# Kernel optimization log

Hardware: AMD Instinct MI355X
Metric: run time of the kernel (lower is better)

The kernel has to match this reference:

```python
import jax, jax.numpy as jnp
import numpy as np

FACTOR = 0.2          # rotation/zoom/shift factor (init kwarg)
SCALE = 1.0 / 255.0   # rescale (init kwarg)
TWO_PI = 6.283185307179586
B, H, W, C = 64, 224, 224, 3


def _reflect(i, n):
    # TF fill_mode='reflect' index mapping (symmetric with edge repeat)
    m = jnp.mod(i, 2 * n)
    return jnp.where(m >= n, 2 * n - 1 - m, m)


def _bilinear(img, xs, ys):
    # img [H,W,C]; xs, ys [H,W] = input-space sample coords for each output pixel
    h, w, _ = img.shape
    x0f = jnp.floor(xs)
    y0f = jnp.floor(ys)
    fx = (xs - x0f)[..., None]
    fy = (ys - y0f)[..., None]
    x0 = x0f.astype(jnp.int32)
    y0 = y0f.astype(jnp.int32)
    x0r = _reflect(x0, w); x1r = _reflect(x0 + 1, w)
    y0r = _reflect(y0, h); y1r = _reflect(y0 + 1, h)
    Ia = img[y0r, x0r]; Ib = img[y0r, x1r]
    Ic = img[y1r, x0r]; Id = img[y1r, x1r]
    top = Ia * (1.0 - fx) + Ib * fx
    bot = Ic * (1.0 - fx) + Id * fx
    return top * (1.0 - fy) + bot * fy


_warp = jax.vmap(_bilinear)  # over batch: images [B,H,W,C], coords [B,H,W]


def setup_inputs() -> dict:
    key = jax.random.key(0)
    k = jax.random.split(key, 5)
    return {
        "image": jax.random.uniform(k[0], (B, H, W, C), jnp.float32) * 255.0,
        "angle_u": jax.random.uniform(k[1], (B,), jnp.float32),
        "zoom_u": jax.random.uniform(k[2], (B, 2), jnp.float32),
        "shift_u": jax.random.uniform(k[3], (B, 2), jnp.float32),
        "flip_u": jax.random.uniform(k[4], (B,), jnp.float32),
    }


def reference(image, angle_u, zoom_u, shift_u, flip_u):
    b, h, w, _ = image.shape
    dt = image.dtype
    yy, xx = jnp.meshgrid(jnp.arange(h, dtype=dt), jnp.arange(w, dtype=dt), indexing='ij')
    cx = (w - 1) / 2.0
    cy = (h - 1) / 2.0

    # 1) rescale
    x = image * SCALE

    # 2) random rotation: angle uniform in [-factor*2pi, +factor*2pi]
    theta = (2.0 * angle_u - 1.0) * FACTOR * TWO_PI            # [B]
    c = jnp.cos(theta)[:, None, None]
    s = jnp.sin(theta)[:, None, None]
    xr = c * (xx - cx) - s * (yy - cy) + cx                    # [B,H,W]
    yr = s * (xx - cx) + c * (yy - cy) + cy
    x = _warp(x, xr, yr)

    # 3) random zoom: zoom factor uniform in [1-factor, 1+factor] per axis
    z = 1.0 + (2.0 * zoom_u - 1.0) * FACTOR                    # [B,2] (h, w)
    zh = z[:, 0][:, None, None]
    zw = z[:, 1][:, None, None]
    xz = zw * (xx - cx) + cx
    yz = zh * (yy - cy) + cy
    x = _warp(x, xz, yz)

    # 4) random translation: shift fraction uniform in [-factor, factor]
    sh = (2.0 * shift_u - 1.0) * FACTOR                        # [B,2] (h, w)
    dy = (sh[:, 0] * h)[:, None, None]
    dx = (sh[:, 1] * w)[:, None, None]
    xt = xx - dx
    yt = yy - dy
    x = _warp(x, xt, yt)

    # 5) random horizontal flip (p = 0.5)
    flip = flip_u > 0.5
    x = jnp.where(flip[:, None, None, None], x[:, :, ::-1, :], x)
    return x
```

## Files before the change

kernel.cpp:

```cpp
#include <hip/hip_runtime.h>
#include <hip/hip_fp16.h>
#include <math.h>

#define BB 64
#define HH 224
#define WW 224
#define CC 3

constexpr float FACTOR  = 0.2f;
constexpr float SCALE_K = 1.0f / 255.0f;
constexpr float TWO_PI_F = 6.283185307179586f;
constexpr float CX = (WW - 1) * 0.5f;
constexpr float CY = (HH - 1) * 0.5f;
constexpr int PIX = HH * WW;
constexpr int IMG_ELEMS = PIX * CC;

constexpr int NXCD = 8;

constexpr int T2X = WW / 32;
constexpr int T2Y = HH / 16;
constexpr int TILES2 = T2X * T2Y;
constexpr int NBLOCKS2 = BB * TILES2;

constexpr int SZP = 50;
constexpr int ZP2 = 34;

typedef float f32x4 __attribute__((ext_vector_type(4), aligned(4)));
typedef float f32x2 __attribute__((ext_vector_type(2), aligned(4)));
typedef unsigned int u32x4 __attribute__((ext_vector_type(4), aligned(8)));

__device__ __forceinline__ int reflect1(int i, int n) {
    i = (i < 0) ? (-1 - i) : i;
    return (i >= n) ? (2 * n - 1 - i) : i;
}

__device__ __forceinline__ void rhull(int a, int b, int n, int& lo, int& hi) {
    int ra = reflect1(a, n), rb = reflect1(b, n);
    lo = min(ra, rb); hi = max(ra, rb);
    if (a <= 0 && b >= -1) lo = 0;
    if (b >= n - 1 && a <= n) hi = n - 1;
}

__device__ __forceinline__ float h2f(unsigned short u) {
    return __half2float(__ushort_as_half(u));
}

__device__ __forceinline__ void decode_tile32(int bid, int& b, int& ox, int& oy) {
    int xcd  = bid & (NXCD - 1);
    int slot = bid >> 3;
    int bi   = slot / TILES2;
    int t    = slot - bi * TILES2;
    b = xcd + bi * NXCD;
    int ty = t / T2X;
    int tx = t - ty * T2X;
    ox = tx * 32; oy = ty * 16;
}

__global__ __launch_bounds__(256)
void rotate_kernel(const float* __restrict__ image, uint2* __restrict__ tmp,
                   const float* __restrict__ angle_u) {
    int b, ox, oy;
    decode_tile32(blockIdx.x, b, ox, oy);
    const int lx = threadIdx.x & 31, ly = threadIdx.x >> 5;
    const int x = ox + lx;

    const float theta = (2.0f * angle_u[b] - 1.0f) * FACTOR * TWO_PI_F;
    const float c = __cosf(theta), s = __sinf(theta);
    const float rx = (float)x - CX;
    const float* img = image + (size_t)b * IMG_ELEMS;

    float fx[2], fy[2];
    bool sA[2], sB[2];
    f32x4 t4[2], b4[2];
    f32x2 t2[2], b2[2];
#pragma unroll
    for (int k = 0; k < 2; ++k) {
        const int y = oy + ly + k * 8;
        const float ry = (float)y - CY;
        const float xs = c * rx - s * ry + CX;
        const float ys = s * rx + c * ry + CY;
        const float x0f = floorf(xs), y0f = floorf(ys);
        fx[k] = xs - x0f; fy[k] = ys - y0f;
        const int x0 = (int)x0f, y0 = (int)y0f;
        const int x0r = reflect1(x0,     WW);
        const int x1r = reflect1(x0 + 1, WW);
        const int y0r = reflect1(y0,     HH);
        const int y1r = reflect1(y0 + 1, HH);
        int xl = min(x0r, x1r); xl = min(xl, WW - 2);
        sA[k] = (x0r != xl);
        sB[k] = (x1r != xl);
        const float* rT = img + (y0r * WW + xl) * CC;
        const float* rB = img + (y1r * WW + xl) * CC;
        t4[k] = *(const f32x4*)rT;
        t2[k] = *(const f32x2*)(rT + 4);
        b4[k] = *(const f32x4*)rB;
        b2[k] = *(const f32x2*)(rB + 4);
    }

#pragma unroll
    for (int k = 0; k < 2; ++k) {
        const int y = oy + ly + k * 8;
        float TA[3] = { sA[k] ? t4[k].w : t4[k].x, sA[k] ? t2[k].x : t4[k].y, sA[k] ? t2[k].y : t4[k].z };
        float TB[3] = { sB[k] ? t4[k].w : t4[k].x, sB[k] ? t2[k].x : t4[k].y, sB[k] ? t2[k].y : t4[k].z };
        float BA[3] = { sA[k] ? b4[k].w : b4[k].x, sA[k] ? b2[k].x : b4[k].y, sA[k] ? b2[k].y : b4[k].z };
        float BC[3] = { sB[k] ? b4[k].w : b4[k].x, sB[k] ? b2[k].x : b4[k].y, sB[k] ? b2[k].y : b4[k].z };
        const float omfx = 1.0f - fx[k], omfy = 1.0f - fy[k];
        float o[3];
#pragma unroll
        for (int ch = 0; ch < CC; ++ch) {
            float top = TA[ch] * omfx + TB[ch] * fx[k];
            float bot = BA[ch] * omfx + BC[ch] * fx[k];
            o[ch] = (top * omfy + bot * fy[k]) * SCALE_K;
        }
        uint2 v;
        v.x = (unsigned)__half_as_ushort(__float2half_rn(o[0])) |
              ((unsigned)__half_as_ushort(__float2half_rn(o[1])) << 16);
        v.y = (unsigned)__half_as_ushort(__float2half_rn(o[2]));
        tmp[(size_t)b * PIX + (size_t)y * WW + x] = v;
    }
}

__global__ __launch_bounds__(256)
void zoomshift_kernel(const uint2* __restrict__ tmp, float* __restrict__ out,
                      const float* __restrict__ zoom_u,
                      const float* __restrict__ shift_u,
                      const float* __restrict__ flip_u) {
    __shared__ uint2  Sz[24 * SZP];
    __shared__ float4 Z[17 * ZP2];
    __shared__ float4 XD[33], YD[17];

    const int tid = threadIdx.x;
    int b, ox, oy;
    decode_tile32(blockIdx.x, b, ox, oy);

    const float zh = 1.0f + (2.0f * zoom_u[2 * b + 0] - 1.0f) * FACTOR;
    const float zw = 1.0f + (2.0f * zoom_u[2 * b + 1] - 1.0f) * FACTOR;
    const float dy = ((2.0f * shift_u[2 * b + 0] - 1.0f) * FACTOR) * (float)HH;
    const float dx = ((2.0f * shift_u[2 * b + 1] - 1.0f) * FACTOR) * (float)WW;
    const bool flip = flip_u[b] > 0.5f;

    const float ndxf = floorf(-dx), ndyf = floorf(-dy);
    const int Kx = (int)ndxf, Ky = (int)ndyf;
    const float fx3 = -dx - ndxf, fy3 = -dy - ndyf;

    const int Xmin = (flip ? WW - 32 - ox : ox) + Kx;
    const int Ymin = oy + Ky;

    int XrLo, XrHi, YrLo, YrHi;
    rhull(Xmin, Xmin + 32, WW, XrLo, XrHi);
    rhull(Ymin, Ymin + 16, HH, YrLo, YrHi);
    const int Gx0 = (int)floorf(zw * ((float)XrLo - CX) + CX);
    const int Gx1 = (int)floorf(zw * ((float)XrHi - CX) + CX) + 1;
    const int Gy0 = (int)floorf(zh * ((float)YrLo - CY) + CY);
    const int Gy1 = (int)floorf(zh * ((float)YrHi - CY) + CY) + 1;
    int Cx0, Cx1, Cy0, Cy1;
    rhull(Gx0, Gx1, WW, Cx0, Cx1);
    rhull(Gy0, Gy1, HH, Cy0, Cy1);
    const int ColBase = max(min(Cx0, WW - 48), 0) & ~1;
    const int RowBase = max(min(Cy0, HH - 24), 0);

    const uint2* timg = tmp + (size_t)b * PIX;
    for (int id = tid; id < 576; id += 256) {
        const int row = id / 24;
        const int g   = id - row * 24;
        u32x4 v = *(const u32x4*)(timg + (size_t)(RowBase + row) * WW + ColBase + g * 2);
        *(u32x4*)(&Sz[row * SZP + g * 2]) = v;
    }

    if (tid < 33) {
        const int Xr = reflect1(Xmin + tid, WW);
        const float xs2 = zw * ((float)Xr - CX) + CX;
        const float xf = floorf(xs2);
        const int x20 = (int)xf;
        const int cA = min(max(reflect1(x20,     WW) - ColBase, 0), 47);
        const int cB = min(max(reflect1(x20 + 1, WW) - ColBase, 0), 47);
        XD[tid] = make_float4(xs2 - xf, __int_as_float(cA), __int_as_float(cB), 0.f);
    } else if (tid >= 64 && tid < 81) {
        const int ey = tid - 64;
        const int Yr = reflect1(Ymin + ey, HH);
        const float ys2 = zh * ((float)Yr - CY) + CY;
        const float yf = floorf(ys2);
        const int y20 = (int)yf;
        const int rA = min(max(reflect1(y20,     HH) - RowBase, 0), 23) * SZP;
        const int rB = min(max(reflect1(y20 + 1, HH) - RowBase, 0), 23) * SZP;
        YD[ey] = make_float4(ys2 - yf, __int_as_float(rA), __int_as_float(rB), 0.f);
    }
    __syncthreads();

    for (int e = tid; e < 17 * 33; e += 256) {
        const int ey = e / 33;
        const int ex = e - ey * 33;
        const float4 xd = XD[ex];
        const float4 yd = YD[ey];
        const int cA = __float_as_int(xd.y), cB = __float_as_int(xd.z);
        const int rA = __float_as_int(yd.y), rB = __float_as_int(yd.z);
        const uint2 va = Sz[rA + cA];
        const uint2 vb = Sz[rA + cB];
        const uint2 vc = Sz[rB + cA];
        const uint2 vd = Sz[rB + cB];
        const float fx2 = xd.x, fy2 = yd.x;
        const float ofx = 1.0f - fx2, ofy = 1.0f - fy2;
        float4 res;
        res.x = (h2f((unsigned short)(va.x & 0xffffu)) * ofx + h2f((unsigned short)(vb.x & 0xffffu)) * fx2) * ofy
              + (h2f((unsigned short)(vc.x & 0xffffu)) * ofx + h2f((unsigned short)(vd.x & 0xffffu)) * fx2) * fy2;
        res.y = (h2f((unsigned short)(va.x >> 16)) * ofx + h2f((unsigned short)(vb.x >> 16)) * fx2) * ofy
              + (h2f((unsigned short)(vc.x >> 16)) * ofx + h2f((unsigned short)(vd.x >> 16)) * fx2) * fy2;
        res.z = (h2f((unsigned short)(va.y & 0xffffu)) * ofx + h2f((unsigned short)(vb.y & 0xffffu)) * fx2) * ofy
              + (h2f((unsigned short)(vc.y & 0xffffu)) * ofx + h2f((unsigned short)(vd.y & 0xffffu)) * fx2) * fy2;
        res.w = 0.f;
        Z[ey * ZP2 + ex] = res;
    }
    __syncthreads();

    const float ofx = 1.0f - fx3, ofy = 1.0f - fy3;
#pragma unroll
    for (int i = 0; i < 2; ++i) {
        const int p  = tid + 256 * i;
        const int lx = p & 31, ly = p >> 5;
        const int ix = flip ? (31 - lx) : lx;
        const float4 A  = Z[ly * ZP2 + ix];
        const float4 Bv = Z[ly * ZP2 + ix + 1];
        const float4 Cv = Z[(ly + 1) * ZP2 + ix];
        const float4 Dv = Z[(ly + 1) * ZP2 + ix + 1];
        float* o = out + ((size_t)b * PIX + (size_t)(oy + ly) * WW + (ox + lx)) * CC;
        o[0] = (A.x * ofx + Bv.x * fx3) * ofy + (Cv.x * ofx + Dv.x * fx3) * fy3;
        o[1] = (A.y * ofx + Bv.y * fx3) * ofy + (Cv.y * ofx + Dv.y * fx3) * fy3;
        o[2] = (A.z * ofx + Bv.z * fx3) * ofy + (Cv.z * ofx + Dv.z * fx3) * fy3;
    }
}

extern "C" void kernel_launch(void* const* d_in, const int* in_sizes, int n_in,
                              void* d_out, int out_size, void* d_ws, size_t ws_size,
                              hipStream_t stream) {
    const float* image   = (const float*)d_in[0];
    const float* angle_u = (const float*)d_in[1];
    const float* zoom_u  = (const float*)d_in[2];
    const float* shift_u = (const float*)d_in[3];
    const float* flip_u  = (const float*)d_in[4];
    float* out = (float*)d_out;

    uint2* tmp = (uint2*)d_ws;

    rotate_kernel<<<NBLOCKS2, 256, 0, stream>>>(image, tmp, angle_u);
    zoomshift_kernel<<<NBLOCKS2, 256, 0, stream>>>(tmp, out, zoom_u, shift_u, flip_u);
}
```

Before: 36.87 us.

## Stage rotated-source window in LDS as fp16 before bilinear sampling in rotate kernel

The rotate kernel now computes the bounding box of source coordinates for each 32x16 output tile and cooperatively loads a fixed 40x38 window of the input into shared memory. It rescales the window and packs it to fp16 while loading. The four bilinear taps are then read from LDS instead of issuing scattered global loads per pixel. The aim is to cut redundant uncoalesced global traffic. In exchange it adds a barrier and staging work, clamps out-of-window indices (which could be incorrect if the rotated footprint exceeds the window), and changes precision by interpolating on fp16-quantized inputs.

```diff
diff --git a/kernel.cpp b/kernel.cpp
--- a/kernel.cpp
+++ b/kernel.cpp
@@ -25,8 +25,10 @@
 constexpr int SZP = 50;
 constexpr int ZP2 = 34;
 
+constexpr int WINW = 40;
+constexpr int WINH = 38;
+
 typedef float f32x4 __attribute__((ext_vector_type(4), aligned(4)));
-typedef float f32x2 __attribute__((ext_vector_type(2), aligned(4)));
 typedef unsigned int u32x4 __attribute__((ext_vector_type(4), aligned(8)));
 
 __device__ __forceinline__ int reflect1(int i, int n) {
@@ -43,6 +45,14 @@
 
 __device__ __forceinline__ float h2f(unsigned short u) {
     return __half2float(__ushort_as_half(u));
+}
+
+__device__ __forceinline__ uint2 pack3(float a, float b, float c) {
+    uint2 v;
+    v.x = (unsigned)__half_as_ushort(__float2half_rn(a)) |
+          ((unsigned)__half_as_ushort(__float2half_rn(b)) << 16);
+    v.y = (unsigned)__half_as_ushort(__float2half_rn(c));
+    return v;
 }
 
 __device__ __forceinline__ void decode_tile32(int bid, int& b, int& ox, int& oy) {
@@ -59,64 +69,77 @@
 __global__ __launch_bounds__(256)
 void rotate_kernel(const float* __restrict__ image, uint2* __restrict__ tmp,
                    const float* __restrict__ angle_u) {
+    __shared__ uint2 SW[WINH * WINW];
+
+    const int tid = threadIdx.x;
     int b, ox, oy;
     decode_tile32(blockIdx.x, b, ox, oy);
-    const int lx = threadIdx.x & 31, ly = threadIdx.x >> 5;
-    const int x = ox + lx;
 
     const float theta = (2.0f * angle_u[b] - 1.0f) * FACTOR * TWO_PI_F;
     const float c = __cosf(theta), s = __sinf(theta);
-    const float rx = (float)x - CX;
+
+    const float rx0 = (float)ox - CX, rx1 = (float)(ox + 31) - CX;
+    const float ry0 = (float)oy - CY, ry1 = (float)(oy + 15) - CY;
+    const float xsmin = fminf(c * rx0, c * rx1) + fminf(-s * ry0, -s * ry1) + CX;
+    const float xsmax = fmaxf(c * rx0, c * rx1) + fmaxf(-s * ry0, -s * ry1) + CX;
+    const float ysmin = fminf(s * rx0, s * rx1) + fminf(c * ry0, c * ry1) + CY;
+    const float ysmax = fmaxf(s * rx0, s * rx1) + fmaxf(c * ry0, c * ry1) + CY;
+    int Cx0, Cx1, Cy0, Cy1;
+    rhull((int)floorf(xsmin), (int)floorf(xsmax) + 1, WW, Cx0, Cx1);
+    rhull((int)floorf(ysmin), (int)floorf(ysmax) + 1, HH, Cy0, Cy1);
+    const int ColBase = min(Cx0 & ~3, WW - WINW);
+    const int RowBase = min(Cy0, HH - WINH);
+
     const float* img = image + (size_t)b * IMG_ELEMS;
-
-    float fx[2], fy[2];
-    bool sA[2], sB[2];
-    f32x4 t4[2], b4[2];
-    f32x2 t2[2], b2[2];
+    for (int id = tid; id < WINH * (WINW / 4); id += 256) {
+        const int r = id / (WINW / 4);
+        const int g = id - r * (WINW / 4);
+        const float* src = img + ((size_t)(RowBase + r) * WW + ColBase + g * 4) * CC;
+        f32x4 v0 = *(const f32x4*)(src);
+        f32x4 v1 = *(const f32x4*)(src + 4);
+        f32x4 v2 = *(const f32x4*)(src + 8);
+        uint2 p0 = pack3(v0.x * SCALE_K, v0.y * SCALE_K, v0.z * SCALE_K);
+        uint2 p1 = pack3(v0.w * SCALE_K, v1.x * SCALE_K, v1.y * SCALE_K);
+        uint2 p2 = pack3(v1.z * SCALE_K, v1.w * SCALE_K, v2.x * SCALE_K);
+        uint2 p3 = pack3(v2.y * SCALE_K, v2.z * SCALE_K, v2.w * SCALE_K);
+        u32x4 q0 = { p0.x, p0.y, p1.x, p1.y };
+        u32x4 q1 = { p2.x, p2.y, p3.x, p3.y };
+        *(u32x4*)(&SW[r * WINW + g * 4])     = q0;
+        *(u32x4*)(&SW[r * WINW + g * 4 + 2]) = q1;
+    }
+    __syncthreads();
+
+    const int lx = tid & 31, lyy = tid >> 5;
+    const int x = ox + lx;
+    const float rxv = (float)x - CX;
 #pragma unroll
     for (int k = 0; k < 2; ++k) {
-        const int y = oy + ly + k * 8;
-        const float ry = (float)y - CY;
-        const float xs = c * rx - s * ry + CX;
-        const float ys = s * rx + c * ry + CY;
-        const float x0f = floorf(xs), y0f = floorf(ys);
-        fx[k] = xs - x0f; fy[k] = ys - y0f;
-        const int x0 = (int)x0f, y0 = (int)y0f;
-        const int x0r = reflect1(x0,     WW);
-        const int x1r = reflect1(x0 + 1, WW);
-        const int y0r = reflect1(y0,     HH);
-        const int y1r = reflect1(y0 + 1, HH);
-        int xl = min(x0r, x1r); xl = min(xl, WW - 2);
-        sA[k] = (x0r != xl);
-        sB[k] = (x1r != xl);
-        const float* rT = img + (y0r * WW + xl) * CC;
-        const float* rB = img + (y1r * WW + xl) * CC;
-        t4[k] = *(const f32x4*)rT;
-        t2[k] = *(const f32x2*)(rT + 4);
-        b4[k] = *(const f32x4*)rB;
-        b2[k] = *(const f32x2*)(rB + 4);
-    }
-
-#pragma unroll
-    for (int k = 0; k < 2; ++k) {
-        const int y = oy + ly + k * 8;
-        float TA[3] = { sA[k] ? t4[k].w : t4[k].x, sA[k] ? t2[k].x : t4[k].y, sA[k] ? t2[k].y : t4[k].z };
-        float TB[3] = { sB[k] ? t4[k].w : t4[k].x, sB[k] ? t2[k].x : t4[k].y, sB[k] ? t2[k].y : t4[k].z };
-        float BA[3] = { sA[k] ? b4[k].w : b4[k].x, sA[k] ? b2[k].x : b4[k].y, sA[k] ? b2[k].y : b4[k].z };
-        float BC[3] = { sB[k] ? b4[k].w : b4[k].x, sB[k] ? b2[k].x : b4[k].y, sB[k] ? b2[k].y : b4[k].z };
-        const float omfx = 1.0f - fx[k], omfy = 1.0f - fy[k];
-        float o[3];
-#pragma unroll
-        for (int ch = 0; ch < CC; ++ch) {
-            float top = TA[ch] * omfx + TB[ch] * fx[k];
-            float bot = BA[ch] * omfx + BC[ch] * fx[k];
-            o[ch] = (top * omfy + bot * fy[k]) * SCALE_K;
-        }
-        uint2 v;
-        v.x = (unsigned)__half_as_ushort(__float2half_rn(o[0])) |
-              ((unsigned)__half_as_ushort(__float2half_rn(o[1])) << 16);
-        v.y = (unsigned)__half_as_ushort(__float2half_rn(o[2]));
-        tmp[(size_t)b * PIX + (size_t)y * WW + x] = v;
+        const int y = oy + lyy + k * 8;
+        const float ryv = (float)y - CY;
+        const float xs = c * rxv - s * ryv + CX;
+        const float ys = s * rxv + c * ryv + CY;
+        const float xf = floorf(xs), yf = floorf(ys);
+        const float fx = xs - xf, fy = ys - yf;
+        const int x0 = (int)xf, y0 = (int)yf;
+        const int c0 = min(max(reflect1(x0,     WW) - ColBase, 0), WINW - 1);
+        const int c1 = min(max(reflect1(x0 + 1, WW) - ColBase, 0), WINW - 1);
+        const int r0 = min(max(reflect1(y0,     HH) - RowBase, 0), WINH - 1);
+        const int r1 = min(max(reflect1(y0 + 1, HH) - RowBase, 0), WINH - 1);
+        const uint2 va = SW[r0 * WINW + c0];
+        const uint2 vb = SW[r0 * WINW + c1];
+        const uint2 vc = SW[r1 * WINW + c0];
+        const uint2 vd = SW[r1 * WINW + c1];
+        const float ofx = 1.0f - fx, ofy = 1.0f - fy;
+        const float o0 =
+            (h2f((unsigned short)(va.x & 0xffffu)) * ofx + h2f((unsigned short)(vb.x & 0xffffu)) * fx) * ofy +
+            (h2f((unsigned short)(vc.x & 0xffffu)) * ofx + h2f((unsigned short)(vd.x & 0xffffu)) * fx) * fy;
+        const float o1 =
+            (h2f((unsigned short)(va.x >> 16)) * ofx + h2f((unsigned short)(vb.x >> 16)) * fx) * ofy +
+            (h2f((unsigned short)(vc.x >> 16)) * ofx + h2f((unsigned short)(vd.x >> 16)) * fx) * fy;
+        const float o2 =
+            (h2f((unsigned short)(va.y & 0xffffu)) * ofx + h2f((unsigned short)(vb.y & 0xffffu)) * fx) * ofy +
+            (h2f((unsigned short)(vc.y & 0xffffu)) * ofx + h2f((unsigned short)(vd.y & 0xffffu)) * fx) * fy;
+        tmp[(size_t)b * PIX + (size_t)y * WW + x] = pack3(o0, o1, o2);
     }
 }
 
```

After: 35.76 us (median of 2 runs). -3.0%, faster.
